# Performance work log

Measured on AMD Instinct MI355X. Metric: run time of the kernel, lower is better.

Reference implementation:

```python
import jax, jax.numpy as jnp
import numpy as np

T, N = 64, 1048576  # bitstream length, number of parallel unary channels


def setup_inputs() -> dict:
    key = jax.random.key(0)
    kbits = jax.random.fold_in(key, 1)
    # unary bitstream: each bit is 0 or 1 (Bernoulli(0.5)); stored as float,
    # matching bstype=torch.float output / int8-on-{0,1} internal math exactly.
    bits = (jax.random.uniform(kbits, (T, N)) < 0.5).astype(jnp.float32)
    trace0 = jnp.zeros((N,), jnp.float32)  # JKFF state, torch inits zeros(1)
    return {"input": bits, "trace0": trace0}


def reference(input, trace0):
    # UnarySqrt with emit=False, mode='unipolar', jk_trace=True.
    # Per torch forward (python precedence: `1 - trace & input` == (1-trace)&input):
    #   output = ((1 - trace) & input) + trace
    #   trace' = JKFF(J=output, K=1)  ->  Q' = J & ~Q = output & (1 - trace)
    # On {0,1} bits, AND == multiply; the add is disjoint so stays exact.
    def step(trace, x):
        out = (1.0 - trace) * x + trace
        trace_next = out * (1.0 - trace)
        return trace_next, out

    _, outs = jax.lax.scan(step, trace0, input)  # outs: [T, N]
    return outs
```

## Files before the change

kernel.cpp:

```cpp
#include <hip/hip_runtime.h>
#include <stdint.h>


typedef float v4f __attribute__((ext_vector_type(4)));
typedef uint32_t v4u __attribute__((ext_vector_type(4)));

__global__ __launch_bounds__(1024) void UnarySqrt_pack(
    const v4f* __restrict__ in,
    const v4f* __restrict__ trace0,
    v4u* __restrict__ ws_lo,
    v4u* __restrict__ ws_hi,
    int stride)
{
    const int idx = blockIdx.x * blockDim.x + threadIdx.x;
    if (idx >= stride) return;

    v4f t0 = trace0[idx];
    uint32_t tr[4];
    #pragma unroll
    for (int j = 0; j < 4; ++j) tr[j] = (t0[j] != 0.0f) ? 1u : 0u;

    v4u lo = {0u, 0u, 0u, 0u};
    #pragma unroll 8
    for (int t = 0; t < 32; ++t) {
        v4f x = __builtin_nontemporal_load(
            &in[(size_t)t * (size_t)stride + (size_t)idx]);
        #pragma unroll
        for (int j = 0; j < 4; ++j) {
            uint32_t xb = (x[j] != 0.0f) ? 1u : 0u;
            lo[j] |= (xb | tr[j]) << t;
            tr[j] = xb & (tr[j] ^ 1u);
        }
    }
    v4u hi = {0u, 0u, 0u, 0u};
    #pragma unroll 8
    for (int t = 32; t < 64; ++t) {
        v4f x = __builtin_nontemporal_load(
            &in[(size_t)t * (size_t)stride + (size_t)idx]);
        #pragma unroll
        for (int j = 0; j < 4; ++j) {
            uint32_t xb = (x[j] != 0.0f) ? 1u : 0u;
            hi[j] |= (xb | tr[j]) << (t - 32);
            tr[j] = xb & (tr[j] ^ 1u);
        }
    }
    ws_lo[idx] = lo;
    ws_hi[idx] = hi;
}

__global__ __launch_bounds__(1024) void UnarySqrt_expand(
    const v4u* __restrict__ ws_lo,
    const v4u* __restrict__ ws_hi,
    v4f* __restrict__ out,
    int stride)
{
    const int idx = blockIdx.x * blockDim.x + threadIdx.x;
    if (idx >= stride) return;

    v4u lo = ws_lo[idx];
    v4u hi = ws_hi[idx];

    #pragma unroll 8
    for (int t = 0; t < 32; ++t) {
        v4f o;
        #pragma unroll
        for (int j = 0; j < 4; ++j)
            o[j] = ((lo[j] >> t) & 1u) ? 1.0f : 0.0f;
        out[(size_t)t * (size_t)stride + (size_t)idx] = o;
    }
    #pragma unroll 8
    for (int t = 32; t < 64; ++t) {
        v4f o;
        #pragma unroll
        for (int j = 0; j < 4; ++j)
            o[j] = ((hi[j] >> (t - 32)) & 1u) ? 1.0f : 0.0f;
        out[(size_t)t * (size_t)stride + (size_t)idx] = o;
    }
}

__global__ __launch_bounds__(1024) void UnarySqrt_kernel(
    const v4f* __restrict__ in, const v4f* __restrict__ trace0,
    v4f* __restrict__ out, int stride)
{
    const int idx = blockIdx.x * blockDim.x + threadIdx.x;
    if (idx >= stride) return;

    v4f tr = trace0[idx];
    v4f x  = __builtin_nontemporal_load(&in[idx]);

    #pragma unroll 8
    for (int t = 0; t < 64; ++t) {
        v4f xn;
        if (t + 1 < 64) {
            xn = __builtin_nontemporal_load(
                &in[(size_t)(t + 1) * (size_t)stride + (size_t)idx]);
        }
        v4f p = x * (1.0f - tr);
        v4f o = tr + p;
        out[(size_t)t * (size_t)stride + (size_t)idx] = o;
        tr = p;
        x = xn;
    }
}

__global__ __launch_bounds__(256) void UnarySqrt_generic(
    const v4f* __restrict__ in, const v4f* __restrict__ trace0,
    v4f* __restrict__ out, int stride, int T)
{
    int idx = blockIdx.x * blockDim.x + threadIdx.x;
    if (idx >= stride) return;
    v4f tr = trace0[idx];
    for (int t = 0; t < T; ++t) {
        v4f x = in[(size_t)t * stride + idx];
        v4f p = x * (1.0f - tr);
        out[(size_t)t * stride + idx] = tr + p;
        tr = p;
    }
}

extern "C" void kernel_launch(void* const* d_in, const int* in_sizes, int n_in,
                              void* d_out, int out_size, void* d_ws, size_t ws_size,
                              hipStream_t stream) {
    const float* bits   = (const float*)d_in[0];
    const float* trace0 = (const float*)d_in[1];

    int N = in_sizes[1];
    int T = in_sizes[0] / N;
    int stride = N / 4;

    size_t ws_needed = (size_t)stride * 2 * sizeof(v4u);

    if (T == 64 && (stride % 1024) == 0 && d_ws && ws_size >= ws_needed) {
        int grid = stride / 1024;
        v4u* ws_lo = (v4u*)d_ws;
        v4u* ws_hi = ws_lo + stride;
        UnarySqrt_pack<<<grid, 1024, 0, stream>>>(
            (const v4f*)bits, (const v4f*)trace0, ws_lo, ws_hi, stride);
        UnarySqrt_expand<<<grid, 1024, 0, stream>>>(
            ws_lo, ws_hi, (v4f*)d_out, stride);
    } else if (T == 64 && (stride % 1024) == 0) {
        int grid = stride / 1024;
        UnarySqrt_kernel<<<grid, 1024, 0, stream>>>(
            (const v4f*)bits, (const v4f*)trace0, (v4f*)d_out, stride);
    } else {
        int block = 256;
        int grid = (stride + block - 1) / block;
        UnarySqrt_generic<<<grid, block, 0, stream>>>(
            (const v4f*)bits, (const v4f*)trace0, (v4f*)d_out, stride, T);
    }
}
```

Before: 425.0 us.

## Flatten expand kernel across time steps and use regular loads in pack

The expand kernel goes from one thread per channel group looping over all 64 time steps to a flat grid. Each block of 256 threads writes 1024 contiguous output vectors for a single time step, reading the packed word from the matching half of the workspace. This gives far more blocks and fully contiguous write streams, which should improve memory-level parallelism on the write-heavy phase. The cost is that each packed word is re-read 32 times from the workspace, though that traffic should mostly hit cache. The pack kernel also drops its nontemporal loads in favour of ordinary loads.

```diff
diff --git a/kernel.cpp b/kernel.cpp
--- a/kernel.cpp
+++ b/kernel.cpp
@@ -23,8 +23,7 @@
     v4u lo = {0u, 0u, 0u, 0u};
     #pragma unroll 8
     for (int t = 0; t < 32; ++t) {
-        v4f x = __builtin_nontemporal_load(
-            &in[(size_t)t * (size_t)stride + (size_t)idx]);
+        v4f x = in[(size_t)t * (size_t)stride + (size_t)idx];
         #pragma unroll
         for (int j = 0; j < 4; ++j) {
             uint32_t xb = (x[j] != 0.0f) ? 1u : 0u;
@@ -35,8 +34,7 @@
     v4u hi = {0u, 0u, 0u, 0u};
     #pragma unroll 8
     for (int t = 32; t < 64; ++t) {
-        v4f x = __builtin_nontemporal_load(
-            &in[(size_t)t * (size_t)stride + (size_t)idx]);
+        v4f x = in[(size_t)t * (size_t)stride + (size_t)idx];
         #pragma unroll
         for (int j = 0; j < 4; ++j) {
             uint32_t xb = (x[j] != 0.0f) ? 1u : 0u;
@@ -48,33 +46,27 @@
     ws_hi[idx] = hi;
 }
 
-__global__ __launch_bounds__(1024) void UnarySqrt_expand(
+__global__ __launch_bounds__(256) void UnarySqrt_expand_flat(
     const v4u* __restrict__ ws_lo,
     const v4u* __restrict__ ws_hi,
     v4f* __restrict__ out,
     int stride)
 {
-    const int idx = blockIdx.x * blockDim.x + threadIdx.x;
-    if (idx >= stride) return;
+    const size_t base = (size_t)blockIdx.x * 1024;
+    const int t = (int)(base / (size_t)stride);
+    const int bit = t & 31;
+    const v4u* __restrict__ half = (t < 32) ? ws_lo : ws_hi;
+    const int idx0 = (int)(base % (size_t)stride);
 
-    v4u lo = ws_lo[idx];
-    v4u hi = ws_hi[idx];
-
-    #pragma unroll 8
-    for (int t = 0; t < 32; ++t) {
+    #pragma unroll
+    for (int k = 0; k < 4; ++k) {
+        const int idx = idx0 + k * 256 + (int)threadIdx.x;
+        v4u w = half[idx];
         v4f o;
         #pragma unroll
         for (int j = 0; j < 4; ++j)
-            o[j] = ((lo[j] >> t) & 1u) ? 1.0f : 0.0f;
-        out[(size_t)t * (size_t)stride + (size_t)idx] = o;
-    }
-    #pragma unroll 8
-    for (int t = 32; t < 64; ++t) {
-        v4f o;
-        #pragma unroll
-        for (int j = 0; j < 4; ++j)
-            o[j] = ((hi[j] >> (t - 32)) & 1u) ? 1.0f : 0.0f;
-        out[(size_t)t * (size_t)stride + (size_t)idx] = o;
+            o[j] = (float)((w[j] >> bit) & 1u);
+        out[base + (size_t)(k * 256) + threadIdx.x] = o;
     }
 }
 
@@ -131,12 +123,16 @@
     size_t ws_needed = (size_t)stride * 2 * sizeof(v4u);
 
     if (T == 64 && (stride % 1024) == 0 && d_ws && ws_size >= ws_needed) {
-        int grid = stride / 1024;
         v4u* ws_lo = (v4u*)d_ws;
         v4u* ws_hi = ws_lo + stride;
-        UnarySqrt_pack<<<grid, 1024, 0, stream>>>(
+
+        int pack_grid = stride / 1024;
+        UnarySqrt_pack<<<pack_grid, 1024, 0, stream>>>(
             (const v4f*)bits, (const v4f*)trace0, ws_lo, ws_hi, stride);
-        UnarySqrt_expand<<<grid, 1024, 0, stream>>>(
+
+        size_t M = (size_t)T * (size_t)stride;
+        int exp_grid = (int)(M / 1024);
+        UnarySqrt_expand_flat<<<exp_grid, 256, 0, stream>>>(
             ws_lo, ws_hi, (v4f*)d_out, stride);
     } else if (T == 64 && (stride % 1024) == 0) {
         int grid = stride / 1024;
```

Measured after the change: 449.1 us. 1.06x slower.
